# Optimization experiments

Measured on AMD Instinct MI355X. Metric: run time of the kernel, lower is better.

## Reference

```python
import jax, jax.numpy as jnp
import numpy as np

R = 16            # DFL bins (reg_max)
C = 80            # num classes
STRIDES = (8, 16, 32)
CONF = 0.25
IOU_T = 0.45
MAX_DET = 300
K_PRE = 1024      # fixed pre-NMS candidate count (static-shape stand-in for torch's boolean mask)
CLS_OFFSET = 4096.0  # > max image coord; class-aware NMS offset (torchvision batched_nms trick)


def setup_inputs() -> dict:
    key = jax.random.key(0)
    k0, k1, k2 = jax.random.split(key, 3)
    B, CH = 16, 4 * R + C
    return {
        "p0": jax.random.normal(k0, (B, CH, 80, 80), jnp.float32),
        "p1": jax.random.normal(k1, (B, CH, 40, 40), jnp.float32),
        "p2": jax.random.normal(k2, (B, CH, 20, 20), jnp.float32),
        "h_img": 640,
        "w_img": 640,
    }


def _decode_level(p, stride):
    # p: (B, 4R+C, H, W)
    B, _, H, W = p.shape
    box_logits = p[:, : 4 * R].reshape(B, 4, R, H * W)
    bins = jnp.arange(R, dtype=p.dtype)
    # DFLIntegral: softmax over bins, expectation -> l,t,r,b distances (in stride units)
    ltrb = jnp.einsum('bkrm,r->bkm', jax.nn.softmax(box_logits, axis=2), bins) * stride  # (B,4,HW)
    yv, xv = jnp.meshgrid(jnp.arange(H, dtype=p.dtype), jnp.arange(W, dtype=p.dtype), indexing='ij')
    cx = (xv.reshape(-1) + 0.5) * stride  # (HW,)
    cy = (yv.reshape(-1) + 0.5) * stride
    x1 = cx[None] - ltrb[:, 0]
    y1 = cy[None] - ltrb[:, 1]
    x2 = cx[None] + ltrb[:, 2]
    y2 = cy[None] + ltrb[:, 3]
    boxes = jnp.stack((x1, y1, x2, y2), axis=2)  # (B, HW, 4)
    scores = jax.nn.sigmoid(p[:, 4 * R:].reshape(B, C, H * W))  # (B, C, HW)
    smax = scores.max(axis=1)      # (B, HW)
    labels = scores.argmax(axis=1)  # (B, HW) int
    return boxes, smax, labels


def _pairwise_iou(b):
    # b: (K, 4) xyxy
    area = (b[:, 2] - b[:, 0]) * (b[:, 3] - b[:, 1])
    lt = jnp.maximum(b[:, None, :2], b[None, :, :2])
    rb = jnp.minimum(b[:, None, 2:], b[None, :, 2:])
    wh = jnp.clip(rb - lt, 0.0)
    inter = wh[..., 0] * wh[..., 1]
    return inter / (area[:, None] + area[None, :] - inter + 1e-7)


def _nms_single(boxes, smax, labels):
    # boxes (A,4), smax (A,), labels (A,)
    s = jnp.where(smax > CONF, smax, -1.0)
    sv, idx = jax.lax.top_k(s, K_PRE)          # score-sorted pre-NMS candidates
    bsel = boxes[idx]                           # (K,4)
    lsel = labels[idx]
    vsel = sv > CONF                            # candidate passes conf filter
    boff = bsel + lsel[:, None].astype(bsel.dtype) * CLS_OFFSET  # class-aware offset
    iou = _pairwise_iou(boff)
    iou = iou * (1.0 - jnp.eye(K_PRE, dtype=iou.dtype))  # no self-suppression

    def step(supp, i):
        keep_i = jnp.logical_and(~supp[i], vsel[i])
        supp = jnp.where(keep_i, supp | (iou[i] > IOU_T), supp)
        return supp, keep_i

    _, keep = jax.lax.scan(step, jnp.zeros(K_PRE, bool), jnp.arange(K_PRE))
    rank = jnp.cumsum(keep) - 1
    slot = jnp.where(keep & (rank < MAX_DET), rank, MAX_DET)  # dump overflow into dummy slot
    boxes_out = jnp.zeros((MAX_DET + 1, 4), bsel.dtype).at[slot].set(bsel)[:MAX_DET]
    scores_out = jnp.zeros((MAX_DET + 1,), sv.dtype).at[slot].set(sv)[:MAX_DET]
    labels_out = jnp.full((MAX_DET + 1,), -1, jnp.int32).at[slot].set(lsel.astype(jnp.int32))[:MAX_DET]
    n = jnp.minimum(keep.sum(), MAX_DET)
    valid_out = jnp.arange(MAX_DET) < n
    return boxes_out, scores_out, labels_out, valid_out


def reference(p0, p1, p2, h_img, w_img):
    parts = [_decode_level(p, s) for p, s in zip((p0, p1, p2), STRIDES)]
    boxes = jnp.concatenate([x[0] for x in parts], axis=1)   # (B, A, 4)
    smax = jnp.concatenate([x[1] for x in parts], axis=1)    # (B, A)
    labels = jnp.concatenate([x[2] for x in parts], axis=1)  # (B, A)
    hi = jnp.array([w_img - 1, h_img - 1, w_img - 1, h_img - 1], boxes.dtype)
    boxes = jnp.clip(boxes, 0.0, hi)
    return jax.vmap(_nms_single)(boxes, smax, labels)
```

## Files before the change

kernel.cpp:

```cpp
#include <hip/hip_runtime.h>
#include <stdint.h>

#define NR 16
#define NC 80
#define NA 8400
#define NB 16
#define KPRE 1024
#define MAXDET 300
#define CONF_T 0.25f
#define IOU_THR 0.45f

__device__ __forceinline__ float read_dim(const void* p) {
  int iv = *(const int*)p;
  return (iv > 0 && iv < (1 << 20)) ? (float)iv : *(const float*)p;
}

__device__ __forceinline__ const float* level_ptr(const float* p0, const float* p1,
                                                  const float* p2, int a, int& HW,
                                                  int& W, float& stride, int& m) {
  if (a < 6400)      { HW = 6400; W = 80; stride = 8.f;  m = a;        return p0; }
  else if (a < 8000) { HW = 1600; W = 40; stride = 16.f; m = a - 6400; return p1; }
  else               { HW = 400;  W = 20; stride = 32.f; m = a - 8000; return p2; }
}

__device__ __forceinline__ uint64_t readlane64(uint64_t v, int lane) {
  uint32_t lo = (uint32_t)__builtin_amdgcn_readlane((int)(uint32_t)v, lane);
  uint32_t hi = (uint32_t)__builtin_amdgcn_readlane((int)(uint32_t)(v >> 32), lane);
  return ((uint64_t)hi << 32) | lo;
}

__global__ __launch_bounds__(64) void k_decode(
    const float* __restrict__ p0, const float* __restrict__ p1,
    const float* __restrict__ p2, const void* __restrict__ hp,
    const void* __restrict__ wp, float4* __restrict__ boxes,
    uint32_t* __restrict__ keys, int* __restrict__ labels) {
  int aid = blockIdx.x * 64 + threadIdx.x;
  int b = aid / NA, a = aid - b * NA;
  int HW, W, m; float stride;
  const float* p = level_ptr(p0, p1, p2, a, HW, W, stride, m);
  const float* base = p + (size_t)b * (4 * NR + NC) * HW + m;

  float d[4];
#pragma unroll
  for (int k = 0; k < 4; ++k) {
    const float* bk = base + (size_t)(k * NR) * HW;
    float v[NR]; float mx = -3.4e38f;
#pragma unroll
    for (int r = 0; r < NR; ++r) { v[r] = bk[(size_t)r * HW]; mx = fmaxf(mx, v[r]); }
    float se = 0.f, sn = 0.f;
#pragma unroll
    for (int r = 0; r < NR; ++r) { float e = expf(v[r] - mx); se += e; sn += e * (float)r; }
    d[k] = sn / se * stride;
  }

  const float* bc = base + (size_t)(4 * NR) * HW;
  float ml = -3.4e38f; int mc = NC;
#pragma unroll 8
  for (int ch = 0; ch < NC; ++ch) {
    float vv = bc[(size_t)ch * HW];
    if (vv > ml) { ml = vv; mc = ch; }
  }

  int y = m / W, x = m - y * W;
  float cx = ((float)x + 0.5f) * stride, cy = ((float)y + 0.5f) * stride;
  float hx = read_dim(wp) - 1.f, hy = read_dim(hp) - 1.f;
  boxes[aid] = make_float4(fminf(fmaxf(cx - d[0], 0.f), hx),
                           fminf(fmaxf(cy - d[1], 0.f), hy),
                           fminf(fmaxf(cx + d[2], 0.f), hx),
                           fminf(fmaxf(cy + d[3], 0.f), hy));
  float smax = 1.f / (1.f + expf(-ml));
  float s = smax > CONF_T ? smax : -1.0f;
  uint32_t bt = __float_as_uint(s);
  keys[aid] = (bt & 0x80000000u) ? ~bt : (bt | 0x80000000u);
  labels[aid] = mc;
}

__global__ __launch_bounds__(1024) void k_selcomp(const uint32_t* __restrict__ keys,
                                                  uint64_t* __restrict__ cmp,
                                                  int* __restrict__ ccount) {
  __shared__ __align__(16) uint32_t skeys[NA];
  __shared__ uint32_t whist[16][256];
  __shared__ uint32_t hsum[256];
  __shared__ int s_t16, s_cnt;
  int img = blockIdx.x, tid = threadIdx.x;
  int w = tid >> 6, lane = tid & 63;
  const uint4* kb4 = (const uint4*)(keys + (size_t)img * NA);
  for (int j = tid; j < NA / 4; j += 1024) ((uint4*)skeys)[j] = kb4[j];
  if (tid == 0) s_cnt = 0;
  for (int j = tid; j < 16 * 256; j += 1024) ((uint32_t*)whist)[j] = 0;
  __syncthreads();

  for (int j = tid; j < NA; j += 1024) {
    uint32_t k = skeys[j];
    if (k >= 0xBE800000u) atomicAdd(&whist[w][(k >> 16) - 0xBE80u], 1u);
  }
  __syncthreads();
  if (tid < 256) {
    uint32_t s = 0;
    for (int i = 0; i < 16; ++i) s += whist[i][tid];
    hsum[tid] = s;
  }
  __syncthreads();
  if (tid < 256) {
    uint32_t s = 0;
    for (int j = tid; j < 256; ++j) s += hsum[j];
    if (s >= KPRE && (s - hsum[tid]) < KPRE) s_t16 = 0xBE80 + tid;
    if (tid == 0 && s < KPRE) s_t16 = 0x407F;
  }
  __syncthreads();
  uint32_t t16 = (uint32_t)s_t16;

  for (int j0 = 0; j0 < NA; j0 += 1024) {
    int j = j0 + tid;
    uint32_t k = (j < NA) ? skeys[j] : 0;
    bool pass = (j < NA) && ((k >> 16) >= t16);
    uint64_t mask = __ballot(pass);
    int pre = __popcll(mask & ((1ull << lane) - 1ull));
    int wc = __popcll(mask);
    int base = 0;
    if (lane == 0) base = wc ? atomicAdd(&s_cnt, wc) : 0;
    base = __shfl(base, 0);
    if (pass)
      cmp[(size_t)img * NA + base + pre] =
          ((uint64_t)k << 32) | (uint64_t)(0xFFFFFFFFu - (uint32_t)j);
  }
  __syncthreads();
  if (tid == 0) ccount[img] = s_cnt;
}

__global__ __launch_bounds__(256) void k_rank2(
    const uint64_t* __restrict__ cmp, const int* __restrict__ ccount,
    const float4* __restrict__ boxes, const int* __restrict__ labels,
    float4* __restrict__ selbox, float4* __restrict__ selboff,
    float* __restrict__ selscore, int* __restrict__ sellab) {
  __shared__ uint64_t sk[2048];
  int img = blockIdx.y;
  int M = ccount[img]; if (M > NA) M = NA;
  if (blockIdx.x * 256 >= M) return;
  int c = blockIdx.x * 256 + threadIdx.x;
  uint64_t kc = (c < M) ? cmp[(size_t)img * NA + c] : 0;
  int rank = 0;
  for (int j0 = 0; j0 < M; j0 += 2048) {
    int nchunk = min(2048, M - j0);
    __syncthreads();
    for (int j = threadIdx.x; j < nchunk; j += 256)
      sk[j] = cmp[(size_t)img * NA + j0 + j];
    __syncthreads();
    if (c < M) {
      int j = 0;
      for (; j + 4 <= nchunk; j += 4) {
        rank += (int)(sk[j] > kc) + (int)(sk[j + 1] > kc) +
                (int)(sk[j + 2] > kc) + (int)(sk[j + 3] > kc);
      }
      for (; j < nchunk; ++j) rank += (int)(sk[j] > kc);
    }
  }
  if (c < M && rank < KPRE) {
    int a = (int)(0xFFFFFFFFu - (uint32_t)kc);
    uint32_t uk = (uint32_t)(kc >> 32);
    uint32_t bits = (uk & 0x80000000u) ? (uk & 0x7FFFFFFFu) : ~uk;
    float s = __uint_as_float(bits);
    int lab = labels[img * NA + a];
    float4 bx = boxes[img * NA + a];
    float off = (float)lab * 4096.0f;
    int o = img * KPRE + rank;
    selbox[o] = bx;
    selboff[o] = make_float4(bx.x + off, bx.y + off, bx.z + off, bx.w + off);
    selscore[o] = s;
    sellab[o] = lab;
  }
}

__global__ __launch_bounds__(256) void k_iou(const float4* __restrict__ selboff,
                                             uint64_t* __restrict__ rowmask) {
  __shared__ float4 bb[KPRE];
  __shared__ float sar[KPRE];
  int img = blockIdx.y;
  for (int j = threadIdx.x; j < KPRE; j += 256) {
    float4 v = selboff[img * KPRE + j];
    bb[j] = v;
    sar[j] = (v.z - v.x) * (v.w - v.y);
  }
  __syncthreads();
  int i = blockIdx.x * 16 + (threadIdx.x & 15);
  int w = threadIdx.x >> 4;
  int rot = w & 3;
  float4 bi = bb[i];
  float ai = sar[i];
  uint64_t bits = 0;
  for (int jj = 0; jj < 64; ++jj) {
    int jb = (jj + rot) & 63;
    int j = w * 64 + jb;
    float4 bj = bb[j];
    float lx = fmaxf(bi.x, bj.x), ly = fmaxf(bi.y, bj.y);
    float rx = fminf(bi.z, bj.z), ry = fminf(bi.w, bj.w);
    float iw = fmaxf(rx - lx, 0.f), ih = fmaxf(ry - ly, 0.f);
    float inter = iw * ih;
    float aj = sar[j];
    float iou = inter / (ai + aj - inter + 1e-7f);
    bits |= (uint64_t)((iou > IOU_THR) && (j != i)) << jb;
  }
  rowmask[(size_t)img * 16384 + (size_t)w * 1024 + i] = bits;
}

__global__ __launch_bounds__(64) void k_scan(
    const uint64_t* __restrict__ rowmask, const float4* __restrict__ selbox,
    const float* __restrict__ selscore, const int* __restrict__ sellab,
    float* __restrict__ out) {
  __shared__ float lsc[KPRE];
  __shared__ uint64_t buf[2][16 * 65];
  __shared__ int keepidx[MAXDET];
  int img = blockIdx.x, lane = threadIdx.x;
  int wsel = lane & 15, q = lane >> 4;
  const uint64_t* g = rowmask + (size_t)img * 16384;

  for (int j = lane; j < KPRE; j += 64) lsc[j] = selscore[img * KPRE + j];

  {
    uint64_t r0[16];
#pragma unroll
    for (int t = 0; t < 16; ++t) r0[t] = g[t * 1024 + lane];
#pragma unroll
    for (int t = 0; t < 16; ++t) buf[0][t * 65 + lane] = r0[t];
  }
  asm volatile("" ::: "memory");

  uint64_t remv = 0;
  int n = 0;
  for (int c = 0; c < 16; ++c) {
    uint64_t rn[16];
    if (c + 1 < 16) {
#pragma unroll
      for (int t = 0; t < 16; ++t) rn[t] = g[t * 1024 + (c + 1) * 64 + lane];
    }
    const uint64_t* B = buf[c & 1];
    uint64_t m = B[c * 65 + lane];
    float sc = lsc[c * 64 + lane];
    uint64_t vmask = __ballot(sc > CONF_T);
    uint64_t cur = readlane64(remv, c) | readlane64(remv, c + 16) |
                   readlane64(remv, c + 32) | readlane64(remv, c + 48);
    uint64_t kmask = 0;
#pragma unroll
    for (int ii = 0; ii < 64; ++ii) {
      if (((vmask >> ii) & 1ull) && !((cur >> ii) & 1ull)) {
        cur |= readlane64(m, ii);
        kmask |= (1ull << ii);
        if (lane == 0 && n < MAXDET) keepidx[n] = c * 64 + ii;
        n++;
      }
    }
    {
      uint64_t acc = 0;
#pragma unroll
      for (int t = 0; t < 16; ++t) {
        int ii = q * 16 + t;
        uint64_t msk = (uint64_t)0 - ((kmask >> ii) & 1ull);
        acc |= B[wsel * 65 + ii] & msk;
      }
      remv |= acc;
    }
    if (!((vmask >> 63) & 1ull) || n >= MAXDET) break;
    if (c + 1 < 16) {
#pragma unroll
      for (int t = 0; t < 16; ++t) buf[(c + 1) & 1][t * 65 + lane] = rn[t];
    }
    asm volatile("" ::: "memory");
  }

  asm volatile("" ::: "memory");
  float* ob = out;
  float* os = out + NB * MAXDET * 4;
  float* ol = out + NB * MAXDET * 5;
  float* ov = out + NB * MAXDET * 6;
  int nk = n < MAXDET ? n : MAXDET;
  for (int s0 = 0; s0 < MAXDET; s0 += 64) {
    int slot = s0 + lane;
    if (slot >= MAXDET) break;
    bool v = slot < nk;
    float4 bx = make_float4(0.f, 0.f, 0.f, 0.f);
    float scv = 0.f, lbv = -1.f;
    if (v) {
      int i = keepidx[slot];
      bx = selbox[img * KPRE + i];
      scv = lsc[i];
      lbv = (float)sellab[img * KPRE + i];
    }
    ((float4*)ob)[img * MAXDET + slot] = bx;
    os[img * MAXDET + slot] = scv;
    ol[img * MAXDET + slot] = lbv;
    ov[img * MAXDET + slot] = v ? 1.0f : 0.0f;
  }
}

extern "C" void kernel_launch(void* const* d_in, const int* in_sizes, int n_in,
                              void* d_out, int out_size, void* d_ws, size_t ws_size,
                              hipStream_t stream) {
  const float* p0 = (const float*)d_in[0];
  const float* p1 = (const float*)d_in[1];
  const float* p2 = (const float*)d_in[2];
  const void* hp = d_in[3];
  const void* wp = d_in[4];

  char* ws = (char*)d_ws;
  float4*   boxes    = (float4*)(ws + 0);
  uint64_t* rowmask  = (uint64_t*)(ws + 0);
  uint32_t* keys     = (uint32_t*)(ws + 2150400);
  int*      labels   = (int*)(ws + 2688000);
  float4*   selbox   = (float4*)(ws + 3225600);
  float4*   selboff  = (float4*)(ws + 3487744);
  float*    selscore = (float*)(ws + 3749888);
  int*      sellab   = (int*)(ws + 3815424);
  int*      ccount   = (int*)(ws + 3880960);
  uint64_t* cmp      = (uint64_t*)(ws + 3881024);

  k_decode<<<(NB * NA) / 64, 64, 0, stream>>>(p0, p1, p2, hp, wp,
                                              boxes, keys, labels);
  k_selcomp<<<NB, 1024, 0, stream>>>(keys, cmp, ccount);
  dim3 rg((NA + 255) / 256, NB);
  k_rank2<<<rg, 256, 0, stream>>>(cmp, ccount, boxes, labels,
                                  selbox, selboff, selscore, sellab);
  dim3 ig(KPRE / 16, NB);
  k_iou<<<ig, 256, 0, stream>>>(selboff, rowmask);
  k_scan<<<NB, 64, 0, stream>>>(rowmask, selbox, selscore, sellab,
                                (float*)d_out);
}
```

Measured before the change: 186.3 us.

## Fuse IoU and NMS scan kernels with last-block-done atomic counter

Merges the IoU bitmask kernel and the greedy NMS scan kernel into one launch. Each block computes its IoU rows, then increments a per-image atomic counter, and the last block to finish for an image runs the scan using reused shared memory. The counter is reset in the decode kernel. This removes one kernel launch and its inter-kernel gap, at the cost of relying on threadfence for global memory visibility and running the serial scan in whichever block finishes last.

```diff
diff --git a/kernel.cpp b/kernel.cpp
--- a/kernel.cpp
+++ b/kernel.cpp
@@ -33,8 +33,10 @@
     const float* __restrict__ p0, const float* __restrict__ p1,
     const float* __restrict__ p2, const void* __restrict__ hp,
     const void* __restrict__ wp, float4* __restrict__ boxes,
-    uint32_t* __restrict__ keys, int* __restrict__ labels) {
+    uint32_t* __restrict__ keys, int* __restrict__ labels,
+    int* __restrict__ done) {
   int aid = blockIdx.x * 64 + threadIdx.x;
+  if (aid < NB) done[aid] = 0;
   int b = aid / NA, a = aid - b * NA;
   int HW, W, m; float stride;
   const float* p = level_ptr(p0, p1, p2, a, HW, W, stride, m);
@@ -171,46 +173,59 @@
   }
 }
 
-__global__ __launch_bounds__(256) void k_iou(const float4* __restrict__ selboff,
-                                             uint64_t* __restrict__ rowmask) {
-  __shared__ float4 bb[KPRE];
-  __shared__ float sar[KPRE];
-  int img = blockIdx.y;
-  for (int j = threadIdx.x; j < KPRE; j += 256) {
+__global__ __launch_bounds__(256) void k_iouscan(
+    const float4* __restrict__ selboff, uint64_t* __restrict__ rowmask,
+    int* __restrict__ done, const float4* __restrict__ selbox,
+    const float* __restrict__ selscore, const int* __restrict__ sellab,
+    float* __restrict__ out) {
+  __shared__ __align__(16) char smem[22016];
+  __shared__ int s_last;
+  int img = blockIdx.y, tid = threadIdx.x;
+
+  float4* bb = (float4*)smem;
+  float* sar = (float*)(smem + 16384);
+  for (int j = tid; j < KPRE; j += 256) {
     float4 v = selboff[img * KPRE + j];
     bb[j] = v;
     sar[j] = (v.z - v.x) * (v.w - v.y);
   }
   __syncthreads();
-  int i = blockIdx.x * 16 + (threadIdx.x & 15);
-  int w = threadIdx.x >> 4;
-  int rot = w & 3;
-  float4 bi = bb[i];
-  float ai = sar[i];
-  uint64_t bits = 0;
-  for (int jj = 0; jj < 64; ++jj) {
-    int jb = (jj + rot) & 63;
-    int j = w * 64 + jb;
-    float4 bj = bb[j];
-    float lx = fmaxf(bi.x, bj.x), ly = fmaxf(bi.y, bj.y);
-    float rx = fminf(bi.z, bj.z), ry = fminf(bi.w, bj.w);
-    float iw = fmaxf(rx - lx, 0.f), ih = fmaxf(ry - ly, 0.f);
-    float inter = iw * ih;
-    float aj = sar[j];
-    float iou = inter / (ai + aj - inter + 1e-7f);
-    bits |= (uint64_t)((iou > IOU_THR) && (j != i)) << jb;
-  }
-  rowmask[(size_t)img * 16384 + (size_t)w * 1024 + i] = bits;
-}
-
-__global__ __launch_bounds__(64) void k_scan(
-    const uint64_t* __restrict__ rowmask, const float4* __restrict__ selbox,
-    const float* __restrict__ selscore, const int* __restrict__ sellab,
-    float* __restrict__ out) {
-  __shared__ float lsc[KPRE];
-  __shared__ uint64_t buf[2][16 * 65];
-  __shared__ int keepidx[MAXDET];
-  int img = blockIdx.x, lane = threadIdx.x;
+  {
+    int i = blockIdx.x * 16 + (tid & 15);
+    int w = tid >> 4;
+    int rot = w & 3;
+    float4 bi = bb[i];
+    float ai = sar[i];
+    uint64_t bits = 0;
+    for (int jj = 0; jj < 64; ++jj) {
+      int jb = (jj + rot) & 63;
+      int j = w * 64 + jb;
+      float4 bj = bb[j];
+      float lx = fmaxf(bi.x, bj.x), ly = fmaxf(bi.y, bj.y);
+      float rx = fminf(bi.z, bj.z), ry = fminf(bi.w, bj.w);
+      float iw = fmaxf(rx - lx, 0.f), ih = fmaxf(ry - ly, 0.f);
+      float inter = iw * ih;
+      float aj = sar[j];
+      float iou = inter / (ai + aj - inter + 1e-7f);
+      bits |= (uint64_t)((iou > IOU_THR) && (j != i)) << jb;
+    }
+    rowmask[(size_t)img * 16384 + (size_t)w * 1024 + i] = bits;
+  }
+
+  __syncthreads();
+  if (tid == 0) {
+    __threadfence();
+    s_last = (atomicAdd(&done[img], 1) == (int)gridDim.x - 1);
+  }
+  __syncthreads();
+  if (!s_last) return;
+  __threadfence();
+  if (tid >= 64) return;
+
+  float* lsc = (float*)smem;
+  uint64_t* buf = (uint64_t*)(smem + 4096);
+  int* keepidx = (int*)(smem + 4096 + 16640);
+  int lane = tid;
   int wsel = lane & 15, q = lane >> 4;
   const uint64_t* g = rowmask + (size_t)img * 16384;
 
@@ -221,7 +236,7 @@
 #pragma unroll
     for (int t = 0; t < 16; ++t) r0[t] = g[t * 1024 + lane];
 #pragma unroll
-    for (int t = 0; t < 16; ++t) buf[0][t * 65 + lane] = r0[t];
+    for (int t = 0; t < 16; ++t) buf[t * 65 + lane] = r0[t];
   }
   asm volatile("" ::: "memory");
 
@@ -233,7 +248,7 @@
 #pragma unroll
       for (int t = 0; t < 16; ++t) rn[t] = g[t * 1024 + (c + 1) * 64 + lane];
     }
-    const uint64_t* B = buf[c & 1];
+    const uint64_t* B = buf + (c & 1) * 1040;
     uint64_t m = B[c * 65 + lane];
     float sc = lsc[c * 64 + lane];
     uint64_t vmask = __ballot(sc > CONF_T);
@@ -261,8 +276,9 @@
     }
     if (!((vmask >> 63) & 1ull) || n >= MAXDET) break;
     if (c + 1 < 16) {
-#pragma unroll
-      for (int t = 0; t < 16; ++t) buf[(c + 1) & 1][t * 65 + lane] = rn[t];
+      uint64_t* Bn = buf + ((c + 1) & 1) * 1040;
+#pragma unroll
+      for (int t = 0; t < 16; ++t) Bn[t * 65 + lane] = rn[t];
     }
     asm volatile("" ::: "memory");
   }
@@ -312,15 +328,15 @@
   int*      sellab   = (int*)(ws + 3815424);
   int*      ccount   = (int*)(ws + 3880960);
   uint64_t* cmp      = (uint64_t*)(ws + 3881024);
+  int*      done     = (int*)(ws + 4956224);
 
   k_decode<<<(NB * NA) / 64, 64, 0, stream>>>(p0, p1, p2, hp, wp,
-                                              boxes, keys, labels);
+                                              boxes, keys, labels, done);
   k_selcomp<<<NB, 1024, 0, stream>>>(keys, cmp, ccount);
   dim3 rg((NA + 255) / 256, NB);
   k_rank2<<<rg, 256, 0, stream>>>(cmp, ccount, boxes, labels,
                                   selbox, selboff, selscore, sellab);
   dim3 ig(KPRE / 16, NB);
-  k_iou<<<ig, 256, 0, stream>>>(selboff, rowmask);
-  k_scan<<<NB, 64, 0, stream>>>(rowmask, selbox, selscore, sellab,
-                                (float*)d_out);
-}
+  k_iouscan<<<ig, 256, 0, stream>>>(selboff, rowmask, done,
+                                    selbox, selscore, sellab, (float*)d_out);
+}
```

Result: slower. 206.8 us (+11.0%).
